# Optimization experiments

Hardware: AMD Instinct MI355X
Metric: run time of the kernel (lower is better)

## Reference

```python
import jax, jax.numpy as jnp
import numpy as np

EPS = 1e-6


def box2corners(box):
    # box (N,5): x, y, w, h, alpha -> corners (N,4,2), CCW starting at (+w/2,+h/2)
    x, y, w, h, a = (box[:, i] for i in range(5))
    dx = jnp.array([0.5, -0.5, -0.5, 0.5], dtype=box.dtype)
    dy = jnp.array([0.5, 0.5, -0.5, -0.5], dtype=box.dtype)
    cx = dx[None, :] * w[:, None]
    cy = dy[None, :] * h[:, None]
    cos, sin = jnp.cos(a)[:, None], jnp.sin(a)[:, None]
    rx = cx * cos - cy * sin + x[:, None]
    ry = cx * sin + cy * cos + y[:, None]
    return jnp.stack([rx, ry], axis=-1)


def box_intersections(c1, c2):
    # Pairwise intersections of the 4 edges of box1 with the 4 edges of box2.
    # c1, c2: (N,4,2) -> points (N,16,2), valid mask (N,16)
    l1 = jnp.concatenate([c1, jnp.roll(c1, -1, axis=1)], axis=-1)[:, :, None, :]  # (N,4,1,4)
    l2 = jnp.concatenate([c2, jnp.roll(c2, -1, axis=1)], axis=-1)[:, None, :, :]  # (N,1,4,4)
    x1, y1, x2, y2 = (l1[..., i] for i in range(4))
    x3, y3, x4, y4 = (l2[..., i] for i in range(4))
    den = (x2 - x1) * (y4 - y3) - (y2 - y1) * (x4 - x3)
    den_safe = jnp.where(den == 0, 1.0, den)
    t = ((x3 - x1) * (y4 - y3) - (y3 - y1) * (x4 - x3)) / den_safe
    u = ((x3 - x1) * (y2 - y1) - (y3 - y1) * (x2 - x1)) / den_safe
    mask = (den != 0) & (t > 0.0) & (t < 1.0) & (u > 0.0) & (u < 1.0)
    px = x1 + t * (x2 - x1)
    py = y1 + t * (y2 - y1)
    pts = jnp.stack([px, py], axis=-1) * mask[..., None]
    N = c1.shape[0]
    return pts.reshape(N, 16, 2), mask.reshape(N, 16)


def corners_in_box(c1, c2):
    # Which corners of box1 lie inside box2, via projection onto box2 edges. (N,4) bool
    a = c2[:, 0:1]
    ab = c2[:, 1:2] - a
    ad = c2[:, 3:4] - a
    am = c1 - a  # (N,4,2)
    p_ab = (am * ab).sum(-1) / (ab * ab).sum(-1)
    p_ad = (am * ad).sum(-1) / (ad * ad).sum(-1)
    tol = 1e-6
    return (p_ab > -tol) & (p_ab < 1 + tol) & (p_ad > -tol) & (p_ad < 1 + tol)


def sorted_poly_area(pts, mask):
    # Sort valid vertices CCW around the valid-vertex mean, pad invalid slots with the
    # first sorted vertex (degenerate edges contribute 0), then shoelace area.
    # pts (N,M,2), mask (N,M) bool -> area (N,)
    maskf = mask.astype(pts.dtype)
    num = jnp.maximum(maskf.sum(-1, keepdims=True), 1.0)  # avoid /0 for empty polygons
    mean = (pts * maskf[..., None]).sum(1, keepdims=True) / num[..., None]
    centered = pts - mean
    ang = jnp.arctan2(centered[..., 1], centered[..., 0])
    ang = jnp.where(mask, ang, 1e9)  # invalid vertices sort last
    order = jnp.argsort(ang, axis=-1)
    sp = jnp.take_along_axis(pts, order[..., None], axis=1)
    sm = jnp.take_along_axis(mask, order, axis=1)
    sp = jnp.where(sm[..., None], sp, sp[:, 0:1])  # pad with first (valid) vertex
    nxt = jnp.roll(sp, -1, axis=1)
    cross = sp[..., 0] * nxt[..., 1] - sp[..., 1] * nxt[..., 0]
    return jnp.abs(cross.sum(-1)) * 0.5


def intersection_area(c1, c2):
    # Differentiable convex-polygon intersection area (Rotated_IoU style):
    # candidate vertices = corners of each box inside the other + edge intersections.
    ipts, imask = box_intersections(c1, c2)
    m1 = corners_in_box(c1, c2)
    m2 = corners_in_box(c2, c1)
    pts = jnp.concatenate([c1, c2, ipts], axis=1)    # (N,24,2)
    mask = jnp.concatenate([m1, m2, imask], axis=1)  # (N,24)
    return sorted_poly_area(pts, mask)


def poly_giou_loss(pred, target, weight):
    areas1 = pred[:, 2] * pred[:, 3]
    areas2 = target[:, 2] * target[:, 3]
    c1 = box2corners(pred)
    c2 = box2corners(target)
    overlap = intersection_area(c1, c2)
    union = areas1 + areas2 - overlap + EPS
    ious = jnp.maximum(overlap / union, EPS)
    # poly_enclose: all 8 corners, all valid
    all_pts = jnp.concatenate([c1, c2], axis=1)  # (N,8,2)
    enclose = sorted_poly_area(all_pts, jnp.ones(all_pts.shape[:2], bool))
    gious = ious - (enclose - union) / enclose
    loss = 1.0 - gious
    # weighted_loss with reduction='mean', avg_factor=None, loss_weight=1.0
    return (loss * weight).mean()


def setup_inputs() -> dict:
    key = jax.random.key(0)
    k1, k2, k3, k4, k5 = jax.random.split(key, 5)
    N = 500000
    xy = jax.random.uniform(k1, (N, 2), dtype=jnp.float32) * 100.0
    wh = jax.random.uniform(k2, (N, 2), dtype=jnp.float32) * 10.0 + 1.0
    ang = (jax.random.uniform(k3, (N, 1), dtype=jnp.float32) - 0.5) * np.float32(np.pi)
    pred = jnp.concatenate([xy, wh, ang], axis=-1)
    noise = jax.random.normal(k4, (N, 5), dtype=jnp.float32) * jnp.array(
        [1.0, 1.0, 0.5, 0.5, 0.1], dtype=jnp.float32)
    target = pred + noise
    target = target.at[:, 2:4].set(jnp.maximum(target[:, 2:4], 0.5))
    weight = jax.random.uniform(k5, (N,), dtype=jnp.float32)
    return {"pred": pred, "target": target, "weight": weight}


def reference(pred, target, weight):
    return poly_giou_loss(pred, target, weight)
```

## Files before the change

kernel.cpp:

```cpp
#include <hip/hip_runtime.h>
#include <math.h>

#define BLOCK 256

__device__ __forceinline__ float fast_rcp(float x) {
    return __builtin_amdgcn_rcpf(x);
}
__device__ __forceinline__ float fsin(float x) {
    return __builtin_amdgcn_sinf(x * 0.15915494309189535f);
}
__device__ __forceinline__ float fcos(float x) {
    return __builtin_amdgcn_cosf(x * 0.15915494309189535f);
}

__device__ __forceinline__ float pseudo_angle(float x, float y) {
    float d = fabsf(x) + fabsf(y);
    float p = (d == 0.f) ? 1.f : x * fast_rcp(d);
    return (y < 0.f) ? (p - 1.f) : (1.f - p);
}

__device__ __forceinline__ float seg_in_aabb_cross(float ax, float ay,
                                                   float bx, float by,
                                                   float hw, float hh) {
    float ex = bx - ax, ey = by - ay;
    float t0 = 0.f, t1 = 1.f;
    bool feas = true;
    {
        bool par = (ex == 0.f);
        float r = fast_rcp(ex);
        float ta = (hw - ax) * r, tb = (-hw - ax) * r;
        float tlo = fminf(ta, tb), thi = fmaxf(ta, tb);
        t0 = par ? t0 : fmaxf(t0, tlo);
        t1 = par ? t1 : fminf(t1, thi);
        feas = feas && (!par || (fabsf(ax) <= hw));
    }
    {
        bool par = (ey == 0.f);
        float r = fast_rcp(ey);
        float ta = (hh - ay) * r, tb = (-hh - ay) * r;
        float tlo = fminf(ta, tb), thi = fmaxf(ta, tb);
        t0 = par ? t0 : fmaxf(t0, tlo);
        t1 = par ? t1 : fminf(t1, thi);
        feas = feas && (!par || (fabsf(ay) <= hh));
    }
    bool valid = feas && (t1 > t0);
    float pax = fmaf(t0, ex, ax), pay = fmaf(t0, ey, ay);
    float pbx = fmaf(t1, ex, ax), pby = fmaf(t1, ey, ay);
    float cr = pax * pby - pay * pbx;
    return valid ? cr : 0.f;
}

__device__ __forceinline__ float seg_in_quad_cross(float ax, float ay,
                                                   float ex, float ey,
                                                   const float* qx,
                                                   const float* qy) {
    float t0 = 0.f, t1 = 1.f;
    bool feas = true;
#pragma unroll
    for (int i = 0; i < 4; ++i) {
        int in_ = (i + 1) & 3;
        float dix = qx[in_] - qx[i], diy = qy[in_] - qy[i];
        float ga = dix * (ay - qy[i]) - diy * (ax - qx[i]);
        float gd = dix * ey - diy * ex;
        bool par = (gd == 0.f);
        float tk = -ga * fast_rcp(gd);
        t0 = (!par && gd > 0.f) ? fmaxf(t0, tk) : t0;
        t1 = (!par && gd < 0.f) ? fminf(t1, tk) : t1;
        feas = feas && (!par || (ga >= 0.f));
    }
    bool valid = feas && (t1 > t0);
    float pax = fmaf(t0, ex, ax), pay = fmaf(t0, ey, ay);
    float pbx = fmaf(t1, ex, ax), pby = fmaf(t1, ey, ay);
    float cr = pax * pby - pay * pbx;
    return valid ? cr : 0.f;
}

__launch_bounds__(BLOCK)
__global__ void giou_kernel(const float* __restrict__ pred,
                            const float* __restrict__ target,
                            const float* __restrict__ weight,
                            float* __restrict__ partials, int N) {
    int tid = threadIdx.x;
    long gi = (long)blockIdx.x * BLOCK + tid;
    int i = (gi < (long)N) ? (int)gi : (N - 1);

    float p[5], q[5];
#pragma unroll
    for (int j = 0; j < 5; ++j) p[j] = pred[i * 5 + j];
#pragma unroll
    for (int j = 0; j < 5; ++j) q[j] = target[i * 5 + j];
    float wgt = weight[i];

    float cq = fcos(q[4]), sq = fsin(q[4]);
    float dang = p[4] - q[4];
    float cd = fcos(dang), sd = fsin(dang);
    float hw = 0.5f * q[2], hh = 0.5f * q[3];
    float dxc = p[0] - q[0], dyc = p[1] - q[1];
    float tx = dxc * cq + dyc * sq;
    float ty = -dxc * sq + dyc * cq;
    float ax_ = 0.5f * p[2] * cd, ay_ = 0.5f * p[2] * sd;
    float bx_ = -0.5f * p[3] * sd, by_ = 0.5f * p[3] * cd;

    float qx[4], qy[4];
    qx[0] = tx + ax_ + bx_; qy[0] = ty + ay_ + by_;
    qx[1] = tx - ax_ + bx_; qy[1] = ty - ay_ + by_;
    qx[2] = tx - ax_ - bx_; qy[2] = ty - ay_ - by_;
    qx[3] = tx + ax_ - bx_; qy[3] = ty + ay_ - by_;

    float s = 0.f;
    s += seg_in_aabb_cross(qx[0], qy[0], qx[1], qy[1], hw, hh);
    s += seg_in_aabb_cross(qx[1], qy[1], qx[2], qy[2], hw, hh);
    s += seg_in_aabb_cross(qx[2], qy[2], qx[3], qy[3], hw, hh);
    s += seg_in_aabb_cross(qx[3], qy[3], qx[0], qy[0], hw, hh);
    float w2 = hw + hw, h2 = hh + hh;
    s += seg_in_quad_cross(hw, -hh, 0.f, h2, qx, qy);
    s += seg_in_quad_cross(hw, hh, -w2, 0.f, qx, qy);
    s += seg_in_quad_cross(-hw, hh, 0.f, -h2, qx, qy);
    s += seg_in_quad_cross(-hw, -hh, w2, 0.f, qx, qy);
    float overlap = 0.5f * fabsf(s);

    float enc;
    {
        float px8[8], py8[8];
#pragma unroll
        for (int j = 0; j < 4; ++j) { px8[j] = qx[j]; py8[j] = qy[j]; }
        px8[4] = hw;  py8[4] = hh;
        px8[5] = -hw; py8[5] = hh;
        px8[6] = -hw; py8[6] = -hh;
        px8[7] = hw;  py8[7] = -hh;
        float ex = 0.f, ey = 0.f;
#pragma unroll
        for (int j = 0; j < 8; ++j) { ex += px8[j]; ey += py8[j]; }
        float mx = ex * 0.125f, my = ey * 0.125f;
        float ang[8];
#pragma unroll
        for (int j = 0; j < 8; ++j) ang[j] = pseudo_angle(px8[j] - mx, py8[j] - my);

#define CE(I, J)                                                   \
        {                                                          \
            bool sw = ang[I] > ang[J];                             \
            float ta = sw ? ang[J] : ang[I];                       \
            float tb = sw ? ang[I] : ang[J];                       \
            ang[I] = ta; ang[J] = tb;                              \
            float txp = sw ? px8[J] : px8[I];                      \
            float typ = sw ? py8[J] : py8[I];                      \
            px8[J] = sw ? px8[I] : px8[J];                         \
            py8[J] = sw ? py8[I] : py8[J];                         \
            px8[I] = txp; py8[I] = typ;                            \
        }
        CE(0,1) CE(2,3) CE(4,5) CE(6,7)
        CE(0,2) CE(1,3) CE(4,6) CE(5,7)
        CE(1,2) CE(5,6)
        CE(0,4) CE(1,5) CE(2,6) CE(3,7)
        CE(2,4) CE(3,5)
        CE(1,2) CE(3,4) CE(5,6)
#undef CE

        float acc2 = 0.f;
#pragma unroll
        for (int k = 0; k < 8; ++k) {
            int kn = (k + 1) & 7;
            acc2 += px8[k] * py8[kn] - py8[k] * px8[kn];
        }
        enc = 0.5f * fabsf(acc2);
    }

    float area1 = p[2] * p[3];
    float area2 = q[2] * q[3];
    float uni = area1 + area2 - overlap + 1e-6f;
    float iou = fmaxf(overlap / uni, 1e-6f);
    float giou = iou - (enc - uni) / enc;
    float loss = (1.f - giou) * wgt;
    if (gi >= (long)N) loss = 0.f;

#pragma unroll
    for (int off = 32; off > 0; off >>= 1)
        loss += __shfl_down(loss, off, 64);
    if ((tid & 63) == 0)
        partials[blockIdx.x * (BLOCK / 64) + (tid >> 6)] = loss;
}

__launch_bounds__(1024)
__global__ void reduce_kernel(const float* __restrict__ partials,
                              float* __restrict__ out, int nparts, float scale) {
    __shared__ float acc[16];
    int tid = threadIdx.x;
    float s = 0.f;
    for (int j = tid; j < nparts; j += 1024) s += partials[j];
#pragma unroll
    for (int off = 32; off > 0; off >>= 1)
        s += __shfl_down(s, off, 64);
    if ((tid & 63) == 0) acc[tid >> 6] = s;
    __syncthreads();
    if (tid == 0) {
        float t = 0.f;
#pragma unroll
        for (int k = 0; k < 16; ++k) t += acc[k];
        out[0] = t * scale;
    }
}

extern "C" void kernel_launch(void* const* d_in, const int* in_sizes, int n_in,
                              void* d_out, int out_size, void* d_ws, size_t ws_size,
                              hipStream_t stream) {
    const float* pred   = (const float*)d_in[0];
    const float* target = (const float*)d_in[1];
    const float* weight = (const float*)d_in[2];
    float* out = (float*)d_out;
    float* ws  = (float*)d_ws;
    int N = in_sizes[0] / 5;

    int nblocks = (N + BLOCK - 1) / BLOCK;
    int nparts = nblocks * (BLOCK / 64);
    giou_kernel<<<nblocks, BLOCK, 0, stream>>>(pred, target, weight, ws, N);
    reduce_kernel<<<1, 1024, 0, stream>>>(ws, out, nparts, 1.0f / (float)N);
}
```

Measured before the change: 82.31 us.

## Fuse final reduction into main kernel via last-block atomic counter

Removes the separate single-block reduce kernel. Each block reduces its waves in shared memory, publishes one block sum with a release store, and increments a global atomic counter. The block that arrives last sums all block sums and writes the scaled mean. The second kernel launch goes away, but a hipMemsetAsync is added to reset the counter, and every block now pays for an atomic plus an extra barrier.

```diff
diff --git a/kernel.cpp b/kernel.cpp
--- a/kernel.cpp
+++ b/kernel.cpp
@@ -79,7 +79,13 @@
 __global__ void giou_kernel(const float* __restrict__ pred,
                             const float* __restrict__ target,
                             const float* __restrict__ weight,
-                            float* __restrict__ partials, int N) {
+                            float* __restrict__ block_sums,
+                            unsigned* __restrict__ counter,
+                            float* __restrict__ out,
+                            int N, int nblocks, float scale) {
+    __shared__ float sacc[BLOCK / 64];
+    __shared__ int is_last;
+
     int tid = threadIdx.x;
     long gi = (long)blockIdx.x * BLOCK + tid;
     int i = (gi < (long)N) ? (int)gi : (N - 1);
@@ -176,27 +182,38 @@
 #pragma unroll
     for (int off = 32; off > 0; off >>= 1)
         loss += __shfl_down(loss, off, 64);
-    if ((tid & 63) == 0)
-        partials[blockIdx.x * (BLOCK / 64) + (tid >> 6)] = loss;
-}
-
-__launch_bounds__(1024)
-__global__ void reduce_kernel(const float* __restrict__ partials,
-                              float* __restrict__ out, int nparts, float scale) {
-    __shared__ float acc[16];
-    int tid = threadIdx.x;
-    float s = 0.f;
-    for (int j = tid; j < nparts; j += 1024) s += partials[j];
-#pragma unroll
-    for (int off = 32; off > 0; off >>= 1)
-        s += __shfl_down(s, off, 64);
-    if ((tid & 63) == 0) acc[tid >> 6] = s;
+    if ((tid & 63) == 0) sacc[tid >> 6] = loss;
     __syncthreads();
+
     if (tid == 0) {
+        float bsum = 0.f;
+#pragma unroll
+        for (int k = 0; k < BLOCK / 64; ++k) bsum += sacc[k];
+        __hip_atomic_store(&block_sums[blockIdx.x], bsum,
+                           __ATOMIC_RELEASE, __HIP_MEMORY_SCOPE_AGENT);
+        unsigned old = __hip_atomic_fetch_add(counter, 1u,
+                                              __ATOMIC_ACQ_REL,
+                                              __HIP_MEMORY_SCOPE_AGENT);
+        is_last = (old == (unsigned)(nblocks - 1)) ? 1 : 0;
+    }
+    __syncthreads();
+
+    if (is_last) {
         float t = 0.f;
-#pragma unroll
-        for (int k = 0; k < 16; ++k) t += acc[k];
-        out[0] = t * scale;
+        for (int j = tid; j < nblocks; j += BLOCK)
+            t += __hip_atomic_load(&block_sums[j],
+                                   __ATOMIC_RELAXED, __HIP_MEMORY_SCOPE_AGENT);
+#pragma unroll
+        for (int off = 32; off > 0; off >>= 1)
+            t += __shfl_down(t, off, 64);
+        if ((tid & 63) == 0) sacc[tid >> 6] = t;
+        __syncthreads();
+        if (tid == 0) {
+            float tot = 0.f;
+#pragma unroll
+            for (int k = 0; k < BLOCK / 64; ++k) tot += sacc[k];
+            out[0] = tot * scale;
+        }
     }
 }
 
@@ -207,11 +224,14 @@
     const float* target = (const float*)d_in[1];
     const float* weight = (const float*)d_in[2];
     float* out = (float*)d_out;
-    float* ws  = (float*)d_ws;
     int N = in_sizes[0] / 5;
 
     int nblocks = (N + BLOCK - 1) / BLOCK;
-    int nparts = nblocks * (BLOCK / 64);
-    giou_kernel<<<nblocks, BLOCK, 0, stream>>>(pred, target, weight, ws, N);
-    reduce_kernel<<<1, 1024, 0, stream>>>(ws, out, nparts, 1.0f / (float)N);
-}
+    float* block_sums = (float*)d_ws;
+    unsigned* counter = (unsigned*)((char*)d_ws + (64 << 10));
+
+    hipMemsetAsync(counter, 0, sizeof(unsigned), stream);
+    giou_kernel<<<nblocks, BLOCK, 0, stream>>>(pred, target, weight,
+                                               block_sums, counter, out,
+                                               N, nblocks, 1.0f / (float)N);
+}
```

Measured after the change: 125.7 us. 1.53x slower.
